# Kernel tuning notes

Hardware: AMD Instinct MI355X
Metric: run time of the kernel (lower is better)

## Reference

```python
import jax, jax.numpy as jnp
import numpy as np

N_NODES = 100000
N_EDGES = 3200000
N_GRAPHS = 1024
F_IN = 4
H = 16


def setup_inputs() -> dict:
    key = jax.random.key(0)
    ks = jax.random.split(key, 12)
    x = jax.random.normal(ks[0], (N_NODES, F_IN), dtype=jnp.float32)
    edge_index = jax.random.randint(ks[1], (2, N_EDGES), 0, N_NODES, dtype=jnp.int64)
    y = jax.random.normal(ks[2], (N_GRAPHS, F_IN), dtype=jnp.float32)
    batch = jnp.sort(jax.random.randint(ks[3], (N_NODES,), 0, N_GRAPHS, dtype=jnp.int64))

    def lin(k, fi, fo):
        s = 1.0 / np.sqrt(fi)
        kw, kb = jax.random.split(k)
        W = jax.random.uniform(kw, (fi, fo), jnp.float32, -s, s)
        b = jax.random.uniform(kb, (fo,), jnp.float32, -s, s)
        return W, b

    W1, b1 = lin(ks[4], F_IN, H)
    W2, b2 = lin(ks[5], H, H)
    W3, b3 = lin(ks[6], H, H)
    fcW1, fcb1 = lin(ks[7], H + 4, H)
    fcW2, fcb2 = lin(ks[8], H, H)
    fcW3, fcb3 = lin(ks[9], H, 1)
    return dict(x=x, edge_index=edge_index, y=y, batch=batch,
                W1=W1, b1=b1, W2=W2, b2=b2, W3=W3, b3=b3,
                fcW1=fcW1, fcb1=fcb1, fcW2=fcW2, fcb2=fcb2, fcW3=fcW3, fcb3=fcb3)


def _gcn_norm(edge_index, n):
    # add self-loops, symmetric normalization (PyG GCNConv default)
    loop = jnp.arange(n, dtype=edge_index.dtype)
    src = jnp.concatenate([edge_index[0], loop])
    dst = jnp.concatenate([edge_index[1], loop])
    deg = jax.ops.segment_sum(jnp.ones_like(dst, dtype=jnp.float32), dst, num_segments=n)
    dinv = jnp.where(deg > 0, jax.lax.rsqrt(deg), 0.0)
    norm = dinv[src] * dinv[dst]  # [E + N]
    return src, dst, norm


def _gcn_conv(x, W, b, src, dst, norm, n):
    h = x @ W                       # [N, out]
    msg = h[src] * norm[:, None]    # gather + scale
    out = jax.ops.segment_sum(msg, dst, num_segments=n)  # scatter-add
    return out + b


def reference(x, edge_index, y, batch, W1, b1, W2, b2, W3, b3,
              fcW1, fcb1, fcW2, fcb2, fcW3, fcb3):
    n = x.shape[0]
    src, dst, norm = _gcn_norm(edge_index, n)
    h = jax.nn.relu(_gcn_conv(x, W1, b1, src, dst, norm, n))
    h = jax.nn.relu(_gcn_conv(h, W2, b2, src, dst, norm, n))
    h = jax.nn.relu(_gcn_conv(h, W3, b3, src, dst, norm, n))
    g = jax.ops.segment_sum(h, batch, num_segments=N_GRAPHS)  # global_add_pool
    g = jnp.concatenate([g, y], axis=1)                       # [G, H+4]
    g = jax.nn.relu(g @ fcW1 + fcb1)
    g = jax.nn.relu(g @ fcW2 + fcb2)
    return g @ fcW3 + fcb3  # [G, 1]
```

## Files before the change

kernel.cpp:

```cpp
#include <hip/hip_runtime.h>
#include <hip/hip_fp16.h>

#define N_NODES 100000
#define N_EDGES 3200000
#define N_GRAPHS 1024
#define F_IN 4
#define H 16

#define NB 256
#define NPB 391
#define CAP 13312
#define CHUNK 4096
#define NBLK ((N_EDGES + CHUNK - 1) / CHUNK)
#define BEPT (CHUNK / 512)
#define EPT_C ((CAP + 1023) / 1024)


__device__ __forceinline__ int lane_id() { return threadIdx.x & 63; }

__device__ __forceinline__ int wave_incl_scan(int v) {
#pragma unroll
    for (int d = 1; d < 64; d <<= 1) {
        int x = __shfl_up(v, d, 64);
        if (lane_id() >= d) v += x;
    }
    return v;
}

union h4u { float2 f2; __half2 h2[2]; };
union h8u { float4 f4; __half2 h2[4]; };


__global__ void k_zero_f(float* __restrict__ p, int n) {
    int i = blockIdx.x * blockDim.x + threadIdx.x;
    if (i < n) p[i] = 0.0f;
}


__global__ __launch_bounds__(512) void k_count(const int* __restrict__ dst,
                                               int* __restrict__ blkCnt, int e) {
    __shared__ int h[NB];
    int t = threadIdx.x;
    for (int q = t; q < NB; q += 512) h[q] = 0;
    __syncthreads();
    int e0 = blockIdx.x * CHUNK;
    int e1 = min(e0 + CHUNK, e);
    for (int i = e0 + t; i < e1; i += 512)
        atomicAdd(&h[dst[i] / NPB], 1);
    __syncthreads();
    for (int q = t; q < NB; q += 512) blkCnt[blockIdx.x * NB + q] = h[q];
}

__global__ __launch_bounds__(1024) void k_colscan(const int* __restrict__ blkCnt,
                                                  int* __restrict__ blkBase,
                                                  int* __restrict__ bucketCnt) {
    __shared__ int ws[16];
    __shared__ int wb[16];
    int b = blockIdx.x;
    int t = threadIdx.x;
    int v = (t < NBLK) ? blkCnt[t * NB + b] : 0;
    int incl = wave_incl_scan(v);
    if (lane_id() == 63) ws[t >> 6] = incl;
    __syncthreads();
    if (t == 0) {
        int acc = 0;
#pragma unroll
        for (int q = 0; q < 16; ++q) { wb[q] = acc; acc += ws[q]; }
    }
    __syncthreads();
    int excl = incl - v + wb[t >> 6];
    if (t < NBLK) blkBase[t * NB + b] = excl;
    if (t == NBLK - 1) bucketCnt[b] = excl + v;
}

__global__ void k_scan_buckets(const int* __restrict__ bucketCnt,
                               int* __restrict__ bucketBase) {
    __shared__ int ws[4];
    __shared__ int wb[4];
    int t = threadIdx.x;
    int v = bucketCnt[t];
    int incl = wave_incl_scan(v);
    if (lane_id() == 63) ws[t >> 6] = incl;
    __syncthreads();
    if (t == 0) {
        int acc = 0;
#pragma unroll
        for (int q = 0; q < 4; ++q) { wb[q] = acc; acc += ws[q]; }
    }
    __syncthreads();
    bucketBase[t] = incl - v + wb[t >> 6];
}

__global__ __launch_bounds__(512) void k_place(const int* __restrict__ src,
                                               const int* __restrict__ dst,
                                               const int* __restrict__ bucketBase,
                                               const int* __restrict__ blkBase,
                                               int* __restrict__ ebuf, int e) {
    __shared__ int cnt[NB];
    __shared__ int st[NB];
    __shared__ int lbase[NB];
    __shared__ int ws[4];
    __shared__ int wb[4];
    __shared__ int lsort[CHUNK];
    __shared__ unsigned short bof[CHUNK];
    int t = threadIdx.x;
    for (int q = t; q < NB; q += 512) {
        cnt[q] = 0;
        lbase[q] = bucketBase[q] + blkBase[blockIdx.x * NB + q];
    }
    __syncthreads();
    int e0 = blockIdx.x * CHUNK;
    int e1 = min(e0 + CHUNK, e);
    int m = e1 - e0;
    int vq[BEPT], bq[BEPT], rq[BEPT];
#pragma unroll
    for (int q = 0; q < BEPT; ++q) {
        int i = e0 + t + q * 512;
        bq[q] = -1;
        if (i < e) {
            int s = src[i];
            int d = dst[i];
            int b = d / NPB;
            int l = d - b * NPB;
            vq[q] = s | (l << 20);
            bq[q] = b;
            rq[q] = atomicAdd(&cnt[b], 1);
        }
    }
    __syncthreads();
    int v = (t < NB) ? cnt[t] : 0;
    int incl = wave_incl_scan(v);
    if (t < NB && lane_id() == 63) ws[t >> 6] = incl;
    __syncthreads();
    if (t == 0) {
        int acc = 0;
#pragma unroll
        for (int q = 0; q < 4; ++q) { wb[q] = acc; acc += ws[q]; }
    }
    __syncthreads();
    if (t < NB) st[t] = incl - v + wb[t >> 6];
    __syncthreads();
#pragma unroll
    for (int q = 0; q < BEPT; ++q) {
        if (bq[q] >= 0) {
            int pos = st[bq[q]] + rq[q];
            lsort[pos] = vq[q];
            bof[pos] = (unsigned short)bq[q];
        }
    }
    __syncthreads();
    for (int i = t; i < m; i += 512) {
        int b2 = bof[i];
        ebuf[lbase[b2] + i - st[b2]] = lsort[i];
    }
}

__global__ __launch_bounds__(1024) void k_csrify(const int* __restrict__ ebuf,
                                                 const int* __restrict__ bucketBase,
                                                 const int* __restrict__ bucketCnt,
                                                 const float* __restrict__ x,
                                                 int* __restrict__ csr,
                                                 int* __restrict__ cursor,
                                                 float* __restrict__ dinv,
                                                 __half* __restrict__ ts0) {
    __shared__ int cnt[NPB];
    __shared__ int st[NPB];
    __shared__ int cnt2[NPB];
    __shared__ float sdv[NPB];
    __shared__ int ws[8];
    __shared__ int wb[8];
    __shared__ int lcsr[CAP];
    int t = threadIdx.x;
    int b = blockIdx.x;
    int base = bucketBase[b];
    int m = bucketCnt[b];
    int nbase = b * NPB;
    for (int q = t; q < NPB; q += 1024) { cnt[q] = 0; cnt2[q] = 0; }
    __syncthreads();

    bool fast = (m <= CAP);
    int vq[EPT_C], rq[EPT_C];
    if (fast) {
#pragma unroll
        for (int c = 0; c < EPT_C; ++c) {
            int idx = t + c * 1024;
            vq[c] = -1;
            if (idx < m) {
                int v = ebuf[base + idx];
                vq[c] = v;
                rq[c] = atomicAdd(&cnt[v >> 20], 1);
            }
        }
    } else {
        for (int i = t; i < m; i += 1024)
            atomicAdd(&cnt[ebuf[base + i] >> 20], 1);
    }
    __syncthreads();
    int v0 = (t < NPB) ? cnt[t] : 0;
    int incl = wave_incl_scan(v0);
    if (t < 448 && lane_id() == 63) ws[t >> 6] = incl;
    __syncthreads();
    if (t == 0) {
        int acc = 0;
#pragma unroll
        for (int q = 0; q < 7; ++q) { wb[q] = acc; acc += ws[q]; }
    }
    __syncthreads();
    if (t < NPB) {
        int s = incl - v0 + wb[t >> 6];
        st[t] = s;
        int node = nbase + t;
        if (node < N_NODES) {
            float dv = rsqrtf((float)cnt[t] + 1.0f);
            sdv[t] = dv;
            dinv[node] = dv;
            cursor[node] = base + s + cnt[t];
        }
    }
    __syncthreads();
    for (int idx = t; idx < NPB * F_IN; idx += 1024) {
        int q = idx >> 2;
        int node = nbase + q;
        if (node < N_NODES)
            ts0[node * F_IN + (idx & 3)] =
                __float2half(sdv[q] * x[node * F_IN + (idx & 3)]);
    }
    if (fast) {
#pragma unroll
        for (int c = 0; c < EPT_C; ++c) {
            int v = vq[c];
            if (v >= 0) lcsr[st[v >> 20] + rq[c]] = v & 0xFFFFF;
        }
        __syncthreads();
        for (int i = t; i < m; i += 1024) csr[base + i] = lcsr[i];
    } else {
        for (int i = t; i < m; i += 1024) {
            int v = ebuf[base + i];
            int l = v >> 20;
            int r = atomicAdd(&cnt2[l], 1);
            csr[base + st[l] + r] = v & 0xFFFFF;
        }
    }
}

__global__ __launch_bounds__(256) void k_fused1(const __half* __restrict__ ts,
                                                const float* __restrict__ dinv,
                                                const int* __restrict__ csr,
                                                const int* __restrict__ cursor,
                                                const float* __restrict__ W,
                                                const float* __restrict__ bias,
                                                __half* __restrict__ ts_out, int n) {
    __shared__ float sW[F_IN * H];
    __shared__ float sagg[16][F_IN];
    __shared__ float sdv[16];
    int t = threadIdx.x;
    if (t < F_IN * H) sW[t] = W[t];
    int i0 = blockIdx.x * 16;
    int i = i0 + t / 16;
    int g = t & 15;
    int k2 = g & 1;
    int w = g >> 1;
    if (i < n) {
        int start = (i == 0) ? 0 : cursor[i - 1];
        int end = cursor[i];
        float ax0 = 0.f, ay0 = 0.f, ax1 = 0.f, ay1 = 0.f;
        int j = start + w;
        for (; j + 8 < end; j += 16) {
            int s0 = csr[j];
            int s1 = csr[j + 8];
            float2 f0 = __half22float2(*(const __half2*)&ts[s0 * F_IN + 2 * k2]);
            float2 f1 = __half22float2(*(const __half2*)&ts[s1 * F_IN + 2 * k2]);
            ax0 += f0.x; ay0 += f0.y;
            ax1 += f1.x; ay1 += f1.y;
        }
        for (; j < end; j += 8) {
            float2 f = __half22float2(*(const __half2*)&ts[csr[j] * F_IN + 2 * k2]);
            ax0 += f.x; ay0 += f.y;
        }
        float sx = ax0 + ax1;
        float sy = ay0 + ay1;
        if (w == 0) {
            float2 f = __half22float2(*(const __half2*)&ts[i * F_IN + 2 * k2]);
            sx += f.x; sy += f.y;
        }
#pragma unroll
        for (int msk = 2; msk < 16; msk <<= 1) {
            sx += __shfl_xor(sx, msk, 64);
            sy += __shfl_xor(sy, msk, 64);
        }
        if (w == 0) {
            float dv = dinv[i];
            int nl = t / 16;
            sagg[nl][2 * k2] = dv * sx;
            sagg[nl][2 * k2 + 1] = dv * sy;
            if (k2 == 0) sdv[nl] = dv;
        }
    }
    __syncthreads();
    int nl = t >> 4;
    int k = t & 15;
    int node = i0 + nl;
    if (node < n) {
        float acc = bias[k];
#pragma unroll
        for (int j = 0; j < F_IN; j++) acc = fmaf(sagg[nl][j], sW[j * H + k], acc);
        float h = fmaxf(acc, 0.0f);
        ts_out[node * H + k] = __float2half(sdv[nl] * h);
    }
}

template <bool POOL>
__global__ __launch_bounds__(256) void k_fused16(const __half* __restrict__ ts,
                                                 const float* __restrict__ dinv,
                                                 const int* __restrict__ csr,
                                                 const int* __restrict__ cursor,
                                                 const float* __restrict__ W,
                                                 const float* __restrict__ bias,
                                                 __half* __restrict__ ts_out,
                                                 const int* __restrict__ batch,
                                                 float* __restrict__ g, int n) {
    __shared__ float sW[H * H];
    __shared__ float sagg[8][H];
    __shared__ float sdv[8];
    int t = threadIdx.x;
    sW[t] = W[t];
    int i0 = blockIdx.x * 8;
    int i = i0 + t / 32;
    int lg = t & 31;
    int k8 = lg & 1;
    int w = lg >> 1;
    if (i < n) {
        int start = (i == 0) ? 0 : cursor[i - 1];
        int end = cursor[i];
        float a[8] = {0.f, 0.f, 0.f, 0.f, 0.f, 0.f, 0.f, 0.f};
        float b2[8] = {0.f, 0.f, 0.f, 0.f, 0.f, 0.f, 0.f, 0.f};
        int j = start + w;
        for (; j + 16 < end; j += 32) {
            int s0 = csr[j];
            int s1 = csr[j + 16];
            h8u u0, u1;
            u0.f4 = *(const float4*)&ts[s0 * H + 8 * k8];
            u1.f4 = *(const float4*)&ts[s1 * H + 8 * k8];
#pragma unroll
            for (int q = 0; q < 4; ++q) {
                float2 f0 = __half22float2(u0.h2[q]);
                float2 f1 = __half22float2(u1.h2[q]);
                a[2 * q] += f0.x; a[2 * q + 1] += f0.y;
                b2[2 * q] += f1.x; b2[2 * q + 1] += f1.y;
            }
        }
        for (; j < end; j += 16) {
            h8u u;
            u.f4 = *(const float4*)&ts[csr[j] * H + 8 * k8];
#pragma unroll
            for (int q = 0; q < 4; ++q) {
                float2 f = __half22float2(u.h2[q]);
                a[2 * q] += f.x; a[2 * q + 1] += f.y;
            }
        }
#pragma unroll
        for (int q = 0; q < 8; ++q) a[q] += b2[q];
        if (w == 0) {
            h8u u;
            u.f4 = *(const float4*)&ts[i * H + 8 * k8];
#pragma unroll
            for (int q = 0; q < 4; ++q) {
                float2 f = __half22float2(u.h2[q]);
                a[2 * q] += f.x; a[2 * q + 1] += f.y;
            }
        }
#pragma unroll
        for (int msk = 2; msk < 32; msk <<= 1) {
#pragma unroll
            for (int q = 0; q < 8; ++q) a[q] += __shfl_xor(a[q], msk, 64);
        }
        if (w == 0) {
            float dv = dinv[i];
            int nl = t / 32;
#pragma unroll
            for (int q = 0; q < 8; ++q) sagg[nl][8 * k8 + q] = dv * a[q];
            if (k8 == 0) sdv[nl] = dv;
        }
    }
    __syncthreads();
    if (t < 128) {
        int nl = t >> 4;
        int k = t & 15;
        int node = i0 + nl;
        if (node < n) {
            float acc = bias[k];
#pragma unroll
            for (int j = 0; j < H; j++) acc = fmaf(sagg[nl][j], sW[j * H + k], acc);
            float h = fmaxf(acc, 0.0f);
            if (POOL) {
                atomicAdd(&g[batch[node] * H + k], h);
            } else {
                ts_out[node * H + k] = __float2half(sdv[nl] * h);
            }
        }
    }
}


__global__ void k_mlp(const float* __restrict__ g, const float* __restrict__ y,
                      const float* __restrict__ fcW1, const float* __restrict__ fcb1,
                      const float* __restrict__ fcW2, const float* __restrict__ fcb2,
                      const float* __restrict__ fcW3, const float* __restrict__ fcb3,
                      float* __restrict__ out, int ngraph) {
    int i = blockIdx.x * blockDim.x + threadIdx.x;
    if (i >= ngraph) return;
    float in[H + 4];
#pragma unroll
    for (int k = 0; k < H; k++) in[k] = g[i * H + k];
#pragma unroll
    for (int k = 0; k < 4; k++) in[H + k] = y[i * 4 + k];
    float z1[H];
#pragma unroll
    for (int o = 0; o < H; o++) {
        float a = fcb1[o];
#pragma unroll
        for (int j = 0; j < H + 4; j++) a += in[j] * fcW1[j * H + o];
        z1[o] = fmaxf(a, 0.0f);
    }
    float z2[H];
#pragma unroll
    for (int o = 0; o < H; o++) {
        float a = fcb2[o];
#pragma unroll
        for (int j = 0; j < H; j++) a += z1[j] * fcW2[j * H + o];
        z2[o] = fmaxf(a, 0.0f);
    }
    float a = fcb3[0];
#pragma unroll
    for (int j = 0; j < H; j++) a += z2[j] * fcW3[j];
    out[i] = a;
}


extern "C" void kernel_launch(void* const* d_in, const int* in_sizes, int n_in,
                              void* d_out, int out_size, void* d_ws, size_t ws_size,
                              hipStream_t stream) {
    const float* x    = (const float*)d_in[0];
    const int*   ei   = (const int*)d_in[1];
    const float* y    = (const float*)d_in[2];
    const int*   bat  = (const int*)d_in[3];
    const float* W1   = (const float*)d_in[4];
    const float* b1   = (const float*)d_in[5];
    const float* W2   = (const float*)d_in[6];
    const float* b2   = (const float*)d_in[7];
    const float* W3   = (const float*)d_in[8];
    const float* b3   = (const float*)d_in[9];
    const float* fcW1 = (const float*)d_in[10];
    const float* fcb1 = (const float*)d_in[11];
    const float* fcW2 = (const float*)d_in[12];
    const float* fcb2 = (const float*)d_in[13];
    const float* fcW3 = (const float*)d_in[14];
    const float* fcb3 = (const float*)d_in[15];
    float* out = (float*)d_out;

    const int* src = ei;
    const int* dst = ei + N_EDGES;

    const int B = 256;
    const int GH = N_GRAPHS * H;
    const int gF1  = (N_NODES + 15) / 16;
    const int gF16 = (N_NODES + 7) / 8;

    char* w = (char*)d_ws;
    size_t off = 0;
    int*    bucketCnt    = (int*)(w + off);    off += (size_t)NB * 4;
    int*    bucketBase   = (int*)(w + off);    off += (size_t)NB * 4;
    int*    blkCnt       = (int*)(w + off);    off += (size_t)NBLK * NB * 4;
    int*    blkBase      = (int*)(w + off);    off += (size_t)NBLK * NB * 4;
    int*    cursor       = (int*)(w + off);    off += (size_t)N_NODES * 4;
    float*  dinv         = (float*)(w + off);  off += (size_t)N_NODES * 4;
    int*    ebuf         = (int*)(w + off);    off += (size_t)N_EDGES * 4;
    int*    csr          = (int*)(w + off);    off += (size_t)N_EDGES * 4;
    __half* ts0          = (__half*)(w + off); off += (size_t)N_NODES * F_IN * 2;
    __half* ts1          = (__half*)(w + off); off += (size_t)N_NODES * H * 2;
    __half* ts2          = (__half*)(w + off); off += (size_t)N_NODES * H * 2;
    float*  g            = (float*)(w + off);  off += (size_t)GH * 4;
    (void)ws_size;

    k_count<<<NBLK, 512, 0, stream>>>(dst, blkCnt, N_EDGES);
    k_colscan<<<NB, 1024, 0, stream>>>(blkCnt, blkBase, bucketCnt);
    k_scan_buckets<<<1, NB, 0, stream>>>(bucketCnt, bucketBase);
    k_place<<<NBLK, 512, 0, stream>>>(src, dst, bucketBase, blkBase, ebuf, N_EDGES);
    k_csrify<<<NB, 1024, 0, stream>>>(ebuf, bucketBase, bucketCnt, x, csr, cursor,
                                      dinv, ts0);

    k_fused1<<<gF1, B, 0, stream>>>(ts0, dinv, csr, cursor, W1, b1, ts1, N_NODES);
    k_fused16<false><<<gF16, B, 0, stream>>>(ts1, dinv, csr, cursor, W2, b2, ts2,
                                             nullptr, nullptr, N_NODES);
    k_zero_f<<<(GH + B - 1) / B, B, 0, stream>>>(g, GH);
    k_fused16<true><<<gF16, B, 0, stream>>>(ts2, dinv, csr, cursor, W3, b3, nullptr,
                                            bat, g, N_NODES);

    k_mlp<<<(N_GRAPHS + B - 1) / B, B, 0, stream>>>(g, y, fcW1, fcb1, fcW2, fcb2,
                                                    fcW3, fcb3, out, N_GRAPHS);
}
```

Measured before the change: 185.6 us.

## Fold bucket scan and pool zeroing into neighbors; shrink per-node thread groups

Removes two small kernel launches by folding the bucket prefix-scan into each block of k_place and k_csrify, and moving the zeroing of the pooled buffer into k_colscan. The GCN aggregation kernels now assign fewer threads per node (4 for layer 1 with full 4-half loads, 8 for layers 2/3) with four independent gathers in flight, so each block covers more nodes. This trades launch overhead and idle lanes on low-degree nodes for redundant scan work per block and less parallelism per node.

```diff
diff --git a/kernel.cpp b/kernel.cpp
--- a/kernel.cpp
+++ b/kernel.cpp
@@ -31,12 +31,6 @@
 union h8u { float4 f4; __half2 h2[4]; };
 
 
-__global__ void k_zero_f(float* __restrict__ p, int n) {
-    int i = blockIdx.x * blockDim.x + threadIdx.x;
-    if (i < n) p[i] = 0.0f;
-}
-
-
 __global__ __launch_bounds__(512) void k_count(const int* __restrict__ dst,
                                                int* __restrict__ blkCnt, int e) {
     __shared__ int h[NB];
@@ -53,11 +47,13 @@
 
 __global__ __launch_bounds__(1024) void k_colscan(const int* __restrict__ blkCnt,
                                                   int* __restrict__ blkBase,
-                                                  int* __restrict__ bucketCnt) {
+                                                  int* __restrict__ bucketCnt,
+                                                  float* __restrict__ g) {
     __shared__ int ws[16];
     __shared__ int wb[16];
     int b = blockIdx.x;
     int t = threadIdx.x;
+    if (t < 64) g[b * 64 + t] = 0.0f;
     int v = (t < NBLK) ? blkCnt[t * NB + b] : 0;
     int incl = wave_incl_scan(v);
     if (lane_id() == 63) ws[t >> 6] = incl;
@@ -73,27 +69,9 @@
     if (t == NBLK - 1) bucketCnt[b] = excl + v;
 }
 
-__global__ void k_scan_buckets(const int* __restrict__ bucketCnt,
-                               int* __restrict__ bucketBase) {
-    __shared__ int ws[4];
-    __shared__ int wb[4];
-    int t = threadIdx.x;
-    int v = bucketCnt[t];
-    int incl = wave_incl_scan(v);
-    if (lane_id() == 63) ws[t >> 6] = incl;
-    __syncthreads();
-    if (t == 0) {
-        int acc = 0;
-#pragma unroll
-        for (int q = 0; q < 4; ++q) { wb[q] = acc; acc += ws[q]; }
-    }
-    __syncthreads();
-    bucketBase[t] = incl - v + wb[t >> 6];
-}
-
 __global__ __launch_bounds__(512) void k_place(const int* __restrict__ src,
                                                const int* __restrict__ dst,
-                                               const int* __restrict__ bucketBase,
+                                               const int* __restrict__ bucketCnt,
                                                const int* __restrict__ blkBase,
                                                int* __restrict__ ebuf, int e) {
     __shared__ int cnt[NB];
@@ -104,10 +82,18 @@
     __shared__ int lsort[CHUNK];
     __shared__ unsigned short bof[CHUNK];
     int t = threadIdx.x;
-    for (int q = t; q < NB; q += 512) {
-        cnt[q] = 0;
-        lbase[q] = bucketBase[q] + blkBase[blockIdx.x * NB + q];
-    }
+    for (int q = t; q < NB; q += 512) cnt[q] = 0;
+    int vb = (t < NB) ? bucketCnt[t] : 0;
+    int ib = wave_incl_scan(vb);
+    if (t < NB && lane_id() == 63) ws[t >> 6] = ib;
+    __syncthreads();
+    if (t == 0) {
+        int acc = 0;
+#pragma unroll
+        for (int q = 0; q < 4; ++q) { wb[q] = acc; acc += ws[q]; }
+    }
+    __syncthreads();
+    if (t < NB) lbase[t] = ib - vb + wb[t >> 6] + blkBase[blockIdx.x * NB + t];
     __syncthreads();
     int e0 = blockIdx.x * CHUNK;
     int e1 = min(e0 + CHUNK, e);
@@ -156,7 +142,6 @@
 }
 
 __global__ __launch_bounds__(1024) void k_csrify(const int* __restrict__ ebuf,
-                                                 const int* __restrict__ bucketBase,
                                                  const int* __restrict__ bucketCnt,
                                                  const float* __restrict__ x,
                                                  int* __restrict__ csr,
@@ -169,14 +154,26 @@
     __shared__ float sdv[NPB];
     __shared__ int ws[8];
     __shared__ int wb[8];
+    __shared__ int sbase;
     __shared__ int lcsr[CAP];
     int t = threadIdx.x;
     int b = blockIdx.x;
-    int base = bucketBase[b];
     int m = bucketCnt[b];
     int nbase = b * NPB;
     for (int q = t; q < NPB; q += 1024) { cnt[q] = 0; cnt2[q] = 0; }
-    __syncthreads();
+    int vb = (t < NB) ? bucketCnt[t] : 0;
+    int ibx = wave_incl_scan(vb);
+    if (t < NB && lane_id() == 63) ws[t >> 6] = ibx;
+    __syncthreads();
+    if (t == 0) {
+        int acc = 0;
+#pragma unroll
+        for (int q = 0; q < 4; ++q) { wb[q] = acc; acc += ws[q]; }
+    }
+    __syncthreads();
+    if (t == b) sbase = ibx - vb + wb[t >> 6];
+    __syncthreads();
+    int base = sbase;
 
     bool fast = (m <= CAP);
     int vq[EPT_C], rq[EPT_C];
@@ -251,61 +248,84 @@
                                                 const float* __restrict__ bias,
                                                 __half* __restrict__ ts_out, int n) {
     __shared__ float sW[F_IN * H];
-    __shared__ float sagg[16][F_IN];
-    __shared__ float sdv[16];
+    __shared__ float sagg[64][F_IN];
+    __shared__ float sdv[64];
     int t = threadIdx.x;
     if (t < F_IN * H) sW[t] = W[t];
-    int i0 = blockIdx.x * 16;
-    int i = i0 + t / 16;
-    int g = t & 15;
-    int k2 = g & 1;
-    int w = g >> 1;
+    int i0 = blockIdx.x * 64;
+    int i = i0 + (t >> 2);
+    int w = t & 3;
     if (i < n) {
         int start = (i == 0) ? 0 : cursor[i - 1];
         int end = cursor[i];
-        float ax0 = 0.f, ay0 = 0.f, ax1 = 0.f, ay1 = 0.f;
+        float a[F_IN] = {0.f, 0.f, 0.f, 0.f};
+        float b[F_IN] = {0.f, 0.f, 0.f, 0.f};
         int j = start + w;
-        for (; j + 8 < end; j += 16) {
+        for (; j + 12 < end; j += 16) {
             int s0 = csr[j];
-            int s1 = csr[j + 8];
-            float2 f0 = __half22float2(*(const __half2*)&ts[s0 * F_IN + 2 * k2]);
-            float2 f1 = __half22float2(*(const __half2*)&ts[s1 * F_IN + 2 * k2]);
-            ax0 += f0.x; ay0 += f0.y;
-            ax1 += f1.x; ay1 += f1.y;
-        }
-        for (; j < end; j += 8) {
-            float2 f = __half22float2(*(const __half2*)&ts[csr[j] * F_IN + 2 * k2]);
-            ax0 += f.x; ay0 += f.y;
-        }
-        float sx = ax0 + ax1;
-        float sy = ay0 + ay1;
+            int s1 = csr[j + 4];
+            int s2 = csr[j + 8];
+            int s3 = csr[j + 12];
+            h4u u0, u1, u2, u3;
+            u0.f2 = *(const float2*)&ts[s0 * F_IN];
+            u1.f2 = *(const float2*)&ts[s1 * F_IN];
+            u2.f2 = *(const float2*)&ts[s2 * F_IN];
+            u3.f2 = *(const float2*)&ts[s3 * F_IN];
+#pragma unroll
+            for (int q = 0; q < 2; ++q) {
+                float2 f0 = __half22float2(u0.h2[q]);
+                float2 f1 = __half22float2(u1.h2[q]);
+                float2 f2 = __half22float2(u2.h2[q]);
+                float2 f3 = __half22float2(u3.h2[q]);
+                a[2 * q] += f0.x + f2.x; a[2 * q + 1] += f0.y + f2.y;
+                b[2 * q] += f1.x + f3.x; b[2 * q + 1] += f1.y + f3.y;
+            }
+        }
+        for (; j < end; j += 4) {
+            h4u u;
+            u.f2 = *(const float2*)&ts[csr[j] * F_IN];
+#pragma unroll
+            for (int q = 0; q < 2; ++q) {
+                float2 f = __half22float2(u.h2[q]);
+                a[2 * q] += f.x; a[2 * q + 1] += f.y;
+            }
+        }
+#pragma unroll
+        for (int q = 0; q < F_IN; ++q) a[q] += b[q];
         if (w == 0) {
-            float2 f = __half22float2(*(const __half2*)&ts[i * F_IN + 2 * k2]);
-            sx += f.x; sy += f.y;
-        }
-#pragma unroll
-        for (int msk = 2; msk < 16; msk <<= 1) {
-            sx += __shfl_xor(sx, msk, 64);
-            sy += __shfl_xor(sy, msk, 64);
+            h4u u;
+            u.f2 = *(const float2*)&ts[i * F_IN];
+#pragma unroll
+            for (int q = 0; q < 2; ++q) {
+                float2 f = __half22float2(u.h2[q]);
+                a[2 * q] += f.x; a[2 * q + 1] += f.y;
+            }
+        }
+#pragma unroll
+        for (int msk = 1; msk < 4; msk <<= 1) {
+#pragma unroll
+            for (int q = 0; q < F_IN; ++q) a[q] += __shfl_xor(a[q], msk, 64);
         }
         if (w == 0) {
             float dv = dinv[i];
-            int nl = t / 16;
-            sagg[nl][2 * k2] = dv * sx;
-            sagg[nl][2 * k2 + 1] = dv * sy;
-            if (k2 == 0) sdv[nl] = dv;
-        }
-    }
-    __syncthreads();
-    int nl = t >> 4;
-    int k = t & 15;
-    int node = i0 + nl;
-    if (node < n) {
-        float acc = bias[k];
-#pragma unroll
-        for (int j = 0; j < F_IN; j++) acc = fmaf(sagg[nl][j], sW[j * H + k], acc);
-        float h = fmaxf(acc, 0.0f);
-        ts_out[node * H + k] = __float2half(sdv[nl] * h);
+            int nl = t >> 2;
+#pragma unroll
+            for (int q = 0; q < F_IN; ++q) sagg[nl][q] = dv * a[q];
+            sdv[nl] = dv;
+        }
+    }
+    __syncthreads();
+    for (int idx = t; idx < 64 * H; idx += 256) {
+        int nl = idx >> 4;
+        int k = idx & 15;
+        int node = i0 + nl;
+        if (node < n) {
+            float acc = bias[k];
+#pragma unroll
+            for (int j = 0; j < F_IN; j++) acc = fmaf(sagg[nl][j], sW[j * H + k], acc);
+            float h = fmaxf(acc, 0.0f);
+            ts_out[node * H + k] = __float2half(sdv[nl] * h);
+        }
     }
 }
 
@@ -320,36 +340,42 @@
                                                  const int* __restrict__ batch,
                                                  float* __restrict__ g, int n) {
     __shared__ float sW[H * H];
-    __shared__ float sagg[8][H];
-    __shared__ float sdv[8];
+    __shared__ float sagg[32][H];
+    __shared__ float sdv[32];
     int t = threadIdx.x;
     sW[t] = W[t];
-    int i0 = blockIdx.x * 8;
-    int i = i0 + t / 32;
-    int lg = t & 31;
+    int i0 = blockIdx.x * 32;
+    int i = i0 + (t >> 3);
+    int lg = t & 7;
     int k8 = lg & 1;
     int w = lg >> 1;
     if (i < n) {
         int start = (i == 0) ? 0 : cursor[i - 1];
         int end = cursor[i];
         float a[8] = {0.f, 0.f, 0.f, 0.f, 0.f, 0.f, 0.f, 0.f};
-        float b2[8] = {0.f, 0.f, 0.f, 0.f, 0.f, 0.f, 0.f, 0.f};
+        float b[8] = {0.f, 0.f, 0.f, 0.f, 0.f, 0.f, 0.f, 0.f};
         int j = start + w;
-        for (; j + 16 < end; j += 32) {
+        for (; j + 12 < end; j += 16) {
             int s0 = csr[j];
-            int s1 = csr[j + 16];
-            h8u u0, u1;
+            int s1 = csr[j + 4];
+            int s2 = csr[j + 8];
+            int s3 = csr[j + 12];
+            h8u u0, u1, u2, u3;
             u0.f4 = *(const float4*)&ts[s0 * H + 8 * k8];
             u1.f4 = *(const float4*)&ts[s1 * H + 8 * k8];
+            u2.f4 = *(const float4*)&ts[s2 * H + 8 * k8];
+            u3.f4 = *(const float4*)&ts[s3 * H + 8 * k8];
 #pragma unroll
             for (int q = 0; q < 4; ++q) {
                 float2 f0 = __half22float2(u0.h2[q]);
                 float2 f1 = __half22float2(u1.h2[q]);
-                a[2 * q] += f0.x; a[2 * q + 1] += f0.y;
-                b2[2 * q] += f1.x; b2[2 * q + 1] += f1.y;
-            }
-        }
-        for (; j < end; j += 16) {
+                float2 f2 = __half22float2(u2.h2[q]);
+                float2 f3 = __half22float2(u3.h2[q]);
+                a[2 * q] += f0.x + f2.x; a[2 * q + 1] += f0.y + f2.y;
+                b[2 * q] += f1.x + f3.x; b[2 * q + 1] += f1.y + f3.y;
+            }
+        }
+        for (; j < end; j += 4) {
             h8u u;
             u.f4 = *(const float4*)&ts[csr[j] * H + 8 * k8];
 #pragma unroll
@@ -359,7 +385,7 @@
             }
         }
 #pragma unroll
-        for (int q = 0; q < 8; ++q) a[q] += b2[q];
+        for (int q = 0; q < 8; ++q) a[q] += b[q];
         if (w == 0) {
             h8u u;
             u.f4 = *(const float4*)&ts[i * H + 8 * k8];
@@ -370,22 +396,22 @@
             }
         }
 #pragma unroll
-        for (int msk = 2; msk < 32; msk <<= 1) {
+        for (int msk = 2; msk < 8; msk <<= 1) {
 #pragma unroll
             for (int q = 0; q < 8; ++q) a[q] += __shfl_xor(a[q], msk, 64);
         }
         if (w == 0) {
             float dv = dinv[i];
-            int nl = t / 32;
+            int nl = t >> 3;
 #pragma unroll
             for (int q = 0; q < 8; ++q) sagg[nl][8 * k8 + q] = dv * a[q];
             if (k8 == 0) sdv[nl] = dv;
         }
     }
     __syncthreads();
-    if (t < 128) {
-        int nl = t >> 4;
-        int k = t & 15;
+    for (int idx = t; idx < 32 * H; idx += 256) {
+        int nl = idx >> 4;
+        int k = idx & 15;
         int node = i0 + nl;
         if (node < n) {
             float acc = bias[k];
@@ -463,13 +489,12 @@
 
     const int B = 256;
     const int GH = N_GRAPHS * H;
-    const int gF1  = (N_NODES + 15) / 16;
-    const int gF16 = (N_NODES + 7) / 8;
+    const int gF1  = (N_NODES + 63) / 64;
+    const int gF16 = (N_NODES + 31) / 32;
 
     char* w = (char*)d_ws;
     size_t off = 0;
     int*    bucketCnt    = (int*)(w + off);    off += (size_t)NB * 4;
-    int*    bucketBase   = (int*)(w + off);    off += (size_t)NB * 4;
     int*    blkCnt       = (int*)(w + off);    off += (size_t)NBLK * NB * 4;
     int*    blkBase      = (int*)(w + off);    off += (size_t)NBLK * NB * 4;
     int*    cursor       = (int*)(w + off);    off += (size_t)N_NODES * 4;
@@ -483,16 +508,13 @@
     (void)ws_size;
 
     k_count<<<NBLK, 512, 0, stream>>>(dst, blkCnt, N_EDGES);
-    k_colscan<<<NB, 1024, 0, stream>>>(blkCnt, blkBase, bucketCnt);
-    k_scan_buckets<<<1, NB, 0, stream>>>(bucketCnt, bucketBase);
-    k_place<<<NBLK, 512, 0, stream>>>(src, dst, bucketBase, blkBase, ebuf, N_EDGES);
-    k_csrify<<<NB, 1024, 0, stream>>>(ebuf, bucketBase, bucketCnt, x, csr, cursor,
-                                      dinv, ts0);
+    k_colscan<<<NB, 1024, 0, stream>>>(blkCnt, blkBase, bucketCnt, g);
+    k_place<<<NBLK, 512, 0, stream>>>(src, dst, bucketCnt, blkBase, ebuf, N_EDGES);
+    k_csrify<<<NB, 1024, 0, stream>>>(ebuf, bucketCnt, x, csr, cursor, dinv, ts0);
 
     k_fused1<<<gF1, B, 0, stream>>>(ts0, dinv, csr, cursor, W1, b1, ts1, N_NODES);
     k_fused16<false><<<gF16, B, 0, stream>>>(ts1, dinv, csr, cursor, W2, b2, ts2,
                                              nullptr, nullptr, N_NODES);
-    k_zero_f<<<(GH + B - 1) / B, B, 0, stream>>>(g, GH);
     k_fused16<true><<<gF16, B, 0, stream>>>(ts2, dinv, csr, cursor, W3, b3, nullptr,
                                             bat, g, N_NODES);
 
```

Result: faster. 165.2 us (-11.0%).
